# Kernel tuning notes

Measured on AMD Instinct MI355X. Metric: run time of the kernel, lower is better.

The kernel has to match this reference:

```python
import jax, jax.numpy as jnp
import numpy as np

# Architecture constants (match init_kwargs)
J_OCT, Q, K = 4, 8, 7
DECIMATION, POOLING, INDEX = 2, 8, 0
NF = K * 2 ** J_OCT            # 112 taps per filter (kernel size / time grid length)
NSC = J_OCT * Q                # 32 wavelet scales (complex filters)
POOL_W = POOLING // DECIMATION ** (INDEX + 1)  # 4


def complex_hermite_interp(xi, xk, m, p):
    # xi: (NF,) time grid; xk: (NSC, K) knots; m, p: (2, K) values/derivatives
    h = jnp.array([[1., 0., -3., 2.], [0., 1., -2., 1.],
                   [0., 0., 3., -2.], [0., 0., -1., 1.]], dtype=xi.dtype)
    xx = jnp.stack([xk[:, :-1], xk[:, 1:]], axis=2)            # (NSC, K-1, 2)
    mm = jnp.stack([m[:, :-1], m[:, 1:]], axis=2)              # (2, K-1, 2)
    pp = jnp.stack([p[:, :-1], p[:, 1:]], axis=2)
    y = jnp.concatenate([mm, pp], axis=2)                      # (2, K-1, 4)
    yh = jnp.einsum('iab,bc->iac', y, h)                       # (2, K-1, 4)
    # normalized position in each knot interval: (NSC, K-1, NF)
    xn = (xi[None, None, :] - xx[:, :, 0:1]) / (xx[:, :, 1:2] - xx[:, :, 0:1])
    mask = ((xn >= 0.) & (xn < 1.)).astype(xi.dtype)
    xp = xn[..., None] ** jnp.arange(4, dtype=xi.dtype)        # (NSC, K-1, NF, 4)
    return jnp.einsum('irf,srtf->ist', yh, xp * mask[..., None])  # (2, NSC, NF)


def get_filters(m, p, scales_delta, knots_base):
    scales = 2. ** (jnp.arange(NSC, dtype=jnp.float32) / np.float32(Q)) + scales_delta
    clipped = jnp.clip(knots_base[None, :] * scales[:, None], 1., float(NF - K))
    knots_sum = jnp.cumsum(clipped, axis=1) - clipped          # exclusive cumsum
    knots = knots_sum - (K // 2) * scales[:, None]             # (NSC, K)
    time_max = np.float32(K * 2 ** (J_OCT - 1))
    time_grid = jnp.linspace(-time_max, time_max, NF)
    mask = jnp.ones((1, K), dtype=jnp.float32).at[0, 0].set(0.).at[0, -1].set(0.)
    m_null = m - jnp.mean(m[:, 1:-1], axis=1, keepdims=True)
    f = complex_hermite_interp(time_grid, knots, m_null * mask, p * mask)  # (2, NSC, NF)
    f = f / jnp.max(f, axis=2, keepdims=True)
    filt_concat = f.reshape(2 * NSC, NF)  # [real; imag] rows, same as tf.concat axis=0
    return jnp.transpose(filt_concat)[:, None, :]              # (NF, 1, 2*NSC) = WIO


def scatter_conv(x, kernel):
    B, C, T = x.shape
    xr = x.reshape(B * C, T, 1)
    xp = jnp.pad(xr, ((0, 0), (NF // 2 - 1, NF // 2 + 1), (0, 0)), mode='symmetric')
    return jax.lax.conv_general_dilated(
        xp, kernel, window_strides=(DECIMATION,), padding='VALID',
        dimension_numbers=('NWC', 'WIO', 'NWC'))                # (B*C, To, 2*NSC)


def reference(x, m, p, scales_delta, knots_base):
    B, C, T = x.shape
    kernel = get_filters(m, p, scales_delta, knots_base)
    x_conv, vjp = jax.vjp(lambda xx: scatter_conv(xx, kernel), x)
    u = jnp.sqrt(jnp.square(x_conv[..., :NSC]) + jnp.square(x_conv[..., NSC:]))  # (B*C, To, NSC)
    out_u = jnp.swapaxes(u.reshape(B, C, NSC, -1), 1, 2)       # (B, NSC, C, To)
    pooled = jax.lax.reduce_window(u, 0., jax.lax.add,
                                   (1, POOL_W, 1), (1, POOL_W, 1), 'VALID') / POOL_W
    pooled = jnp.swapaxes(pooled, 1, 2)                        # (B*C, NSC, Tp)
    out_s = pooled.reshape(B, C, NSC, -1)                      # (B, C, NSC, Tp)
    # embedded tf.gradients auxiliary reconstruction loss
    inverse = vjp(x_conv)[0]
    loss = jnp.mean(jnp.square(inverse - jax.lax.stop_gradient(x)))
    return out_u, out_s, loss


def setup_inputs() -> dict:
    key = jax.random.key(0)
    B, C, T = 16, 3, 65536
    x = jax.random.normal(key, (B, C, T), dtype=jnp.float32)
    n = jnp.arange(K, dtype=jnp.float32)
    ham = 0.54 - 0.46 * jnp.cos(2. * jnp.pi * n / K)           # periodic hamming (tf default)
    alt = jnp.cos(n * jnp.pi) * ham
    m = jnp.stack([alt, jnp.zeros(K, jnp.float32)])
    p = jnp.stack([jnp.zeros(K, jnp.float32), alt])
    scales_delta = jnp.zeros(NSC, dtype=jnp.float32)
    knots_base = jnp.ones(K, dtype=jnp.float32)
    return {'x': x, 'm': m, 'p': p, 'scales_delta': scales_delta, 'knots_base': knots_base}
```

## Files before the change

### kernel.cpp

```cpp
#include <hip/hip_runtime.h>

#define TLEN 65536
#define XPLEN 65648
#define TO 32769
#define OU_SIZE 50333184

typedef __attribute__((ext_vector_type(8))) short short8v;
typedef __attribute__((ext_vector_type(4))) float float4v;

__device__ __forceinline__ float fetch_xp(const float* __restrict__ xr, int idx) {
    int p = idx - 55;
    p = (p < 0) ? (-1 - p) : p;
    p = (p >= TLEN) ? (2 * TLEN - 1 - p) : p;
    return xr[p];
}

__device__ __forceinline__ ushort f2bf(float f) {
    unsigned u = __float_as_uint(f);
    unsigned r = (u + 0x7fffu + ((u >> 16) & 1u)) >> 16;
    return (ushort)r;
}

__global__ __launch_bounds__(256) void k1_filters(
    const float* __restrict__ m, const float* __restrict__ p,
    const float* __restrict__ sd, const float* __restrict__ kb,
    float* __restrict__ Wout, ushort* __restrict__ Wtb)
{
    __shared__ float knots[32][8];
    __shared__ float yh[2][6][4];
    __shared__ float fv[2][32][112];
    __shared__ float mx[64];
    __shared__ float mv[2][7], pv[2][7];
    int tid = threadIdx.x;
    if (tid < 32) {
        float s = exp2f((float)tid * 0.125f) + sd[tid];
        float cum = 0.f;
        for (int k = 0; k < 7; ++k) {
            float c = fminf(fmaxf(kb[k] * s, 1.f), 105.f);
            knots[tid][k] = cum - 3.f * s;
            cum += c;
        }
    }
    if (tid < 2) {
        float mean = 0.f;
        for (int k = 1; k <= 5; ++k) mean += m[tid * 7 + k];
        mean *= 0.2f;
        for (int k = 0; k < 7; ++k) {
            float msk = (k == 0 || k == 6) ? 0.f : 1.f;
            mv[tid][k] = (m[tid * 7 + k] - mean) * msk;
            pv[tid][k] = p[tid * 7 + k] * msk;
        }
    }
    __syncthreads();
    if (tid < 12) {
        int i = tid / 6, kk = tid % 6;
        float y0 = mv[i][kk], y1 = mv[i][kk + 1], y2 = pv[i][kk], y3 = pv[i][kk + 1];
        yh[i][kk][0] = y0;
        yh[i][kk][1] = y1;
        yh[i][kk][2] = -3.f * y0 - 2.f * y1 + 3.f * y2 - y3;
        yh[i][kk][3] = 2.f * y0 + y1 - 2.f * y2 + y3;
    }
    __syncthreads();
    for (int idx = tid; idx < 7168; idx += 256) {
        int i = idx / 3584, s = (idx / 112) % 32, fi = idx % 112;
        float xi = -56.f + (float)fi * (112.f / 111.f);
        float val = 0.f;
        for (int kk = 0; kk < 6; ++kk) {
            float x0 = knots[s][kk], x1 = knots[s][kk + 1];
            float xn = (xi - x0) / (x1 - x0);
            if (xn >= 0.f && xn < 1.f) {
                val += ((yh[i][kk][3] * xn + yh[i][kk][2]) * xn + yh[i][kk][1]) * xn + yh[i][kk][0];
            }
        }
        fv[i][s][fi] = val;
    }
    __syncthreads();
    if (tid < 64) {
        int i = tid >> 5, s = tid & 31;
        float mm_ = -1e30f;
        for (int fi = 0; fi < 112; ++fi) mm_ = fmaxf(mm_, fv[i][s][fi]);
        mx[tid] = mm_;
    }
    __syncthreads();
    for (int idx = tid; idx < 7168; idx += 256) {
        int i = idx / 3584, s = (idx / 112) % 32, fi = idx % 112;
        int o = i * 32 + s;
        Wout[fi * 64 + o] = fv[i][s][fi] / mx[o];
    }
    for (int idx = tid; idx < 8192; idx += 256) {
        int o = idx >> 7, k = idx & 127;
        float val = (k < 112) ? fv[o >> 5][o & 31][k] / mx[o] : 0.f;
        Wtb[idx] = f2bf(val);
    }
}

__global__ __launch_bounds__(256) void k1b_A(const float* __restrict__ W, float* __restrict__ A)
{
    int idx = blockIdx.x * 256 + threadIdx.x;
    if (idx >= 12544) return;
    int j = idx / 112, k = idx % 112;
    float s = 0.f;
    for (int o = 0; o < 64; ++o) s += W[j * 64 + o] * W[k * 64 + o];
    A[idx] = s;
}

__global__ __launch_bounds__(256) void k1c_C(const float* __restrict__ A, float* __restrict__ C)
{
    int idx = blockIdx.x * 256 + threadIdx.x;
    if (idx >= 448) return;
    int q = idx / 224, dd = idx % 224;
    int d = dd - 111;
    float s = 0.f;
    for (int k = q; k < 112; k += 2) {
        int jj = k + d;
        if (jj >= 0 && jj < 112) s += A[jj * 112 + k];
    }
    C[idx] = s;
}

__global__ __launch_bounds__(256) void k2_fwd(
    const float* __restrict__ x, const ushort* __restrict__ Wtb,
    float* __restrict__ out_u, float* __restrict__ out_s)
{
    __shared__ __align__(16) ushort xraw[2][384];
    __shared__ float ub[256][33];
    __shared__ float pb[32][65];
    int row = blockIdx.y;
    int b = row / 3, c = row % 3;
    const float* xr = x + row * TLEN;
    int tid = threadIdx.x;
    int l = tid & 63, w = tid >> 6;
    int r16 = l & 15, kg = l >> 4;

    union U8 { short8v v; uint u[4]; uint4 q; };

    const ushort* WB = Wtb + r16 * 128 + 8 * kg;
    U8 wreg[4][4];
#pragma unroll
    for (int n = 0; n < 4; ++n)
#pragma unroll
        for (int ks = 0; ks < 4; ++ks)
            wreg[n][ks].q = *(const uint4*)(WB + n * 2048 + 32 * ks);

    int ebase = 2 * (32 * w + r16) + 8 * kg;

    int tstart = blockIdx.x * 8;
    int tend = (blockIdx.x == 31) ? 257 : (tstart + 8);

    for (int tile = tstart; tile < tend; ++tile) {
        int half = (tile - tstart) & 1;
        int t0 = tile * 128;

        for (int i = tid; i < 384; i += 256) {
            int idx = 2 * t0 + i;
            float v = (idx < XPLEN) ? fetch_xp(xr, idx) : 0.f;
            xraw[half][i] = f2bf(v);
        }
        __syncthreads();

        float4v acc[2][4];
#pragma unroll
        for (int mt = 0; mt < 2; ++mt)
#pragma unroll
            for (int n = 0; n < 4; ++n)
                acc[mt][n] = (float4v){0.f, 0.f, 0.f, 0.f};

#pragma unroll
        for (int ks = 0; ks < 4; ++ks) {
            U8 a0, a1;
            int e0 = ebase + 32 * ks;
#pragma unroll
            for (int q = 0; q < 4; ++q) {
                a0.u[q] = *(const uint*)&xraw[half][e0 + 2 * q];
                a1.u[q] = *(const uint*)&xraw[half][e0 + 32 + 2 * q];
            }
#pragma unroll
            for (int n = 0; n < 4; ++n) {
                acc[0][n] = __builtin_amdgcn_mfma_f32_16x16x32_bf16(a0.v, wreg[n][ks].v, acc[0][n], 0, 0, 0);
                acc[1][n] = __builtin_amdgcn_mfma_f32_16x16x32_bf16(a1.v, wreg[n][ks].v, acc[1][n], 0, 0, 0);
            }
        }

#pragma unroll
        for (int mt = 0; mt < 2; ++mt) {
            int tl = 32 * w + 16 * mt + 4 * kg;
            int ts = t0 + tl;
            float u1[4], u2[4];
#pragma unroll
            for (int r = 0; r < 4; ++r) {
                float re1 = acc[mt][0][r], im1 = acc[mt][2][r];
                float re2 = acc[mt][1][r], im2 = acc[mt][3][r];
                u1[r] = sqrtf(re1 * re1 + im1 * im1);
                u2[r] = sqrtf(re2 * re2 + im2 * im2);
            }
#pragma unroll
            for (int r = 0; r < 4; ++r) {
                ub[(half << 7) + tl + r][r16]      = u1[r];
                ub[(half << 7) + tl + r][r16 + 16] = u2[r];
            }
            if (ts + 3 < TO) {
                int pc = (tl >> 2) + (half << 5);
                pb[r16][pc]      = (u1[0] + u1[1] + u1[2] + u1[3]) * 0.25f;
                pb[r16 + 16][pc] = (u2[0] + u2[1] + u2[2] + u2[3]) * 0.25f;
            }
        }

        if (half || tile == tend - 1) {
            __syncthreads();
            int nt = half ? 2 : 1;
            int pend_t0 = (tile - nt + 1) * 128;
            int NE = nt << 7;

            for (int i = tid; i < (NE << 3); i += 256) {
                int r = i & 31;
                int g = i >> 5;
                size_t gb = ((size_t)((b * 32 + r) * 3 + c)) * TO + pend_t0;
                int pad = (int)((4 - (gb & 3)) & 3);
                int e = pad + (g << 2);
                if (e + 3 < NE) {
                    int t = pend_t0 + e;
                    float4 v = make_float4(ub[e][r], ub[e + 1][r], ub[e + 2][r], ub[e + 3][r]);
                    if (t + 3 < TO) {
                        *(float4*)(out_u + gb + e) = v;
                    } else {
                        if (t     < TO) out_u[gb + e]     = v.x;
                        if (t + 1 < TO) out_u[gb + e + 1] = v.y;
                        if (t + 2 < TO) out_u[gb + e + 2] = v.z;
                        if (t + 3 < TO) out_u[gb + e + 3] = v.w;
                    }
                }
            }
            if (tid < 128) {
                int r = tid >> 2, j = tid & 3;
                size_t gb = ((size_t)((b * 32 + r) * 3 + c)) * TO + pend_t0;
                int pad = (int)((4 - (gb & 3)) & 3);
                if (pad > 0) {
                    int G4 = ((NE - pad) >> 2) << 2;
                    int e = (j < pad) ? j : (pad + G4 + (j - pad));
                    if (e < NE) {
                        int t = pend_t0 + e;
                        if (t < TO) out_u[gb + e] = ub[e][r];
                    }
                }
            }
            int tp0 = pend_t0 >> 2;
            for (int i = tid; i < (nt << 8); i += 256) {
                int r = i & 31;
                int g = i >> 5;
                int tp = tp0 + (g << 2);
                size_t sb = ((size_t)(row * 32 + r)) * 8192;
                if (tp + 3 < 8192) {
                    float4 v = make_float4(pb[r][4 * g], pb[r][4 * g + 1], pb[r][4 * g + 2], pb[r][4 * g + 3]);
                    *(float4*)(out_s + sb + tp) = v;
                } else {
#pragma unroll
                    for (int j = 0; j < 4; ++j)
                        if (tp + j < 8192) out_s[sb + tp + j] = pb[r][4 * g + j];
                }
            }
        }
    }
}

__global__ __launch_bounds__(256) void k3_interior(
    const float* __restrict__ x, const float* __restrict__ C,
    double* __restrict__ part)
{
    __shared__ __align__(16) float sx[1248];
    __shared__ __align__(16) float Cl[448];
    __shared__ double wred[4];
    int row = blockIdx.y;
    int s0 = 56 + blockIdx.x * 1024;
    const float* xr = x + row * TLEN;
    int tid = threadIdx.x;
    for (int li = tid; li < 1248; li += 256) {
        int pp = s0 - 111 + li;
        pp = (pp < 0) ? (-1 - pp) : pp;
        pp = (pp >= TLEN) ? (2 * TLEN - 1 - pp) : pp;
        sx[li] = xr[pp];
    }
    for (int li = tid; li < 448; li += 256) Cl[li] = C[li];
    __syncthreads();

    int qe = (55 + s0) & 1;
    const float* Ce = Cl + qe * 224;
    const float* Co = Cl + (qe ^ 1) * 224;
    int base = tid * 4;
    float a0 = 0.f, a1 = 0.f, a2 = 0.f, a3 = 0.f;
    float4 cur = *(const float4*)&sx[base];
#pragma unroll 4
    for (int d4 = 0; d4 < 56; ++d4) {
        float4 nxt = *(const float4*)&sx[base + 4 * d4 + 4];
        float4 cev = *(const float4*)&Ce[4 * d4];
        float4 cov = *(const float4*)&Co[4 * d4];
        a0 = fmaf(cur.x, cev.x, a0); a1 = fmaf(cur.y, cov.x, a1); a2 = fmaf(cur.z, cev.x, a2); a3 = fmaf(cur.w, cov.x, a3);
        a0 = fmaf(cur.y, cev.y, a0); a1 = fmaf(cur.z, cov.y, a1); a2 = fmaf(cur.w, cev.y, a2); a3 = fmaf(nxt.x, cov.y, a3);
        a0 = fmaf(cur.z, cev.z, a0); a1 = fmaf(cur.w, cov.z, a1); a2 = fmaf(nxt.x, cev.z, a2); a3 = fmaf(nxt.y, cov.z, a3);
        a0 = fmaf(cur.w, cev.w, a0); a1 = fmaf(nxt.x, cov.w, a1); a2 = fmaf(nxt.y, cev.w, a2); a3 = fmaf(nxt.z, cov.w, a3);
        cur = nxt;
    }

    int sb = s0 + base;
    double lsum = 0.0;
    if (sb + 0 <= 65478) { float d = a0 - sx[base + 111]; lsum += (double)d * d; }
    if (sb + 1 <= 65478) { float d = a1 - sx[base + 112]; lsum += (double)d * d; }
    if (sb + 2 <= 65478) { float d = a2 - sx[base + 113]; lsum += (double)d * d; }
    if (sb + 3 <= 65478) { float d = a3 - sx[base + 114]; lsum += (double)d * d; }
    for (int off = 32; off > 0; off >>= 1) lsum += __shfl_down(lsum, off, 64);
    int w = tid >> 6;
    if ((tid & 63) == 0) wred[w] = lsum;
    __syncthreads();
    if (tid == 0)
        part[row * 64 + blockIdx.x] = wred[0] + wred[1] + wred[2] + wred[3];
}

__global__ __launch_bounds__(256) void k4_edge(
    const float* __restrict__ x, const float* __restrict__ A,
    double* __restrict__ part2)
{
    __shared__ float Al[112][113];
    __shared__ float xpw[240];
    __shared__ double wacc[4];
    int row = blockIdx.x >> 1;
    int side = blockIdx.x & 1;
    const float* xr = x + row * TLEN;
    int tid = threadIdx.x;

    for (int idx = tid; idx < 12544; idx += 256)
        Al[idx / 112][idx % 112] = A[idx];
    {
        int n_x = side ? 225 : 222;
        int woff0 = side ? 65423 : 0;
        if (tid < n_x) xpw[tid] = fetch_xp(xr, woff0 + tid);
    }
    __syncthreads();

    int w = tid >> 6, lane = tid & 63;
    int nS = side ? 57 : 56;
    int woff = side ? 65423 : 0;
    double lacc = 0.0;
    for (int s = w; s < nS; s += 4) {
        float part = 0.f;
#pragma unroll
        for (int half = 0; half < 2; ++half) {
            int i;
            bool has;
            if (!side) { i = half ? (54 - s) : (55 + s); has = half ? (s <= 54) : true; }
            else       { i = half ? (65647 - s) : (65534 + s); has = true; }
            if (has) {
                int klo = max(0, i - 65536);
                int khi = min(111, i);
                int k0 = klo + ((klo ^ i) & 1);
                for (int k = k0; k <= khi; k += 2) {
                    int bi = i - k - woff;
                    part = fmaf(xpw[bi + lane], Al[lane][k], part);
                    if (lane < 48)
                        part = fmaf(xpw[bi + 64 + lane], Al[lane + 64][k], part);
                }
            }
        }
        for (int off = 32; off > 0; off >>= 1) part += __shfl_down(part, off, 64);
        if (lane == 0) {
            float xs = xpw[side ? (111 + s) : (s + 55)];
            float diff = part - xs;
            lacc += (double)diff * diff;
        }
    }
    if (lane == 0) wacc[w] = lacc;
    __syncthreads();
    if (tid == 0) part2[blockIdx.x] = wacc[0] + wacc[1] + wacc[2] + wacc[3];
}

__global__ __launch_bounds__(256) void k5_final(
    const double* __restrict__ part, const double* __restrict__ part2,
    float* __restrict__ out_loss)
{
    __shared__ double red[256];
    double acc = 0.0;
    for (int idx = threadIdx.x; idx < 3072; idx += 256) acc += part[idx];
    if (threadIdx.x < 96) acc += part2[threadIdx.x];
    red[threadIdx.x] = acc;
    __syncthreads();
    for (int st = 128; st > 0; st >>= 1) {
        if (threadIdx.x < st) red[threadIdx.x] += red[threadIdx.x + st];
        __syncthreads();
    }
    if (threadIdx.x == 0)
        out_loss[0] = (float)(red[0] / 3145728.0);
}

extern "C" void kernel_launch(void* const* d_in, const int* in_sizes, int n_in,
                              void* d_out, int out_size, void* d_ws, size_t ws_size,
                              hipStream_t stream)
{
    (void)in_sizes; (void)n_in; (void)ws_size;
    const float* x  = (const float*)d_in[0];
    const float* m  = (const float*)d_in[1];
    const float* p  = (const float*)d_in[2];
    const float* sd = (const float*)d_in[3];
    const float* kb = (const float*)d_in[4];
    float* out = (float*)d_out;
    float* ws  = (float*)d_ws;

    float* ws_w     = ws;
    float* ws_C     = ws + 7168;
    float* ws_A     = ws + 7616;
    double* ws_part  = (double*)(ws + 20160);
    double* ws_part2 = (double*)(ws + 26304);
    ushort* ws_wtb  = (ushort*)(ws + 26496);

    k1_filters<<<1, 256, 0, stream>>>(m, p, sd, kb, ws_w, ws_wtb);
    k1b_A<<<49, 256, 0, stream>>>(ws_w, ws_A);
    k1c_C<<<2, 256, 0, stream>>>(ws_A, ws_C);
    k2_fwd<<<dim3(32, 48), 256, 0, stream>>>(x, ws_wtb, out, out + OU_SIZE);
    k3_interior<<<dim3(64, 48), 256, 0, stream>>>(x, ws_C, ws_part);
    k4_edge<<<96, 256, 0, stream>>>(x, ws_A, ws_part2);
    k5_final<<<1, 256, 0, stream>>>(ws_part, ws_part2, out + (out_size - 1));
}
```

Before: 279.7 us.

## Software-pipeline conv tile loop: prefetch next input and flush previous tile's outputs

Restructures the MFMA convolution tile loop so global loads for the next tile's input are issued before the current tile's compute. The previous tile's output stores (modulus and pooled rows) are flushed per tile, interleaved with that prefetch, rather than in bursts every two tiles. Custom LDS-only barriers with sched_barrier fences replace __syncthreads to keep the compiler from reordering across stages. The aim is to hide global load latency and spread store traffic, at the cost of more barriers per tile and smaller 128-element store batches.

```diff
diff --git a/kernel.cpp b/kernel.cpp
--- a/kernel.cpp
+++ b/kernel.cpp
@@ -19,6 +19,13 @@
     unsigned u = __float_as_uint(f);
     unsigned r = (u + 0x7fffu + ((u >> 16) & 1u)) >> 16;
     return (ushort)r;
+}
+
+__device__ __forceinline__ void bar_lds() {
+    __builtin_amdgcn_sched_barrier(0);
+    asm volatile("s_waitcnt lgkmcnt(0)" ::: "memory");
+    __builtin_amdgcn_s_barrier();
+    __builtin_amdgcn_sched_barrier(0);
 }
 
 __global__ __launch_bounds__(256) void k1_filters(
@@ -146,18 +153,99 @@
 
     int tstart = blockIdx.x * 8;
     int tend = (blockIdx.x == 31) ? 257 : (tstart + 8);
-
-    for (int tile = tstart; tile < tend; ++tile) {
-        int half = (tile - tstart) & 1;
-        int t0 = tile * 128;
-
-        for (int i = tid; i < 384; i += 256) {
-            int idx = 2 * t0 + i;
-            float v = (idx < XPLEN) ? fetch_xp(xr, idx) : 0.f;
-            xraw[half][i] = f2bf(v);
-        }
-        __syncthreads();
-
+    int ntiles = tend - tstart;
+
+    auto flush = [&](int f) {
+        int slot = (f & 1) << 7;
+        int pend_t0 = (tstart + f) * 128;
+        const int NE = 128;
+        for (int i = tid; i < (NE << 3); i += 256) {
+            int r = i & 31;
+            int g = i >> 5;
+            size_t gb = ((size_t)((b * 32 + r) * 3 + c)) * TO + pend_t0;
+            int pad = (int)((4 - (gb & 3)) & 3);
+            int e = pad + (g << 2);
+            if (e + 3 < NE) {
+                int t = pend_t0 + e;
+                float4 v = make_float4(ub[slot + e][r], ub[slot + e + 1][r],
+                                       ub[slot + e + 2][r], ub[slot + e + 3][r]);
+                if (t + 3 < TO) {
+                    *(float4*)(out_u + gb + e) = v;
+                } else {
+                    if (t     < TO) out_u[gb + e]     = v.x;
+                    if (t + 1 < TO) out_u[gb + e + 1] = v.y;
+                    if (t + 2 < TO) out_u[gb + e + 2] = v.z;
+                    if (t + 3 < TO) out_u[gb + e + 3] = v.w;
+                }
+            }
+        }
+        if (tid < 128) {
+            int r = tid >> 2, j = tid & 3;
+            size_t gb = ((size_t)((b * 32 + r) * 3 + c)) * TO + pend_t0;
+            int pad = (int)((4 - (gb & 3)) & 3);
+            if (pad > 0) {
+                int G4 = ((NE - pad) >> 2) << 2;
+                int e = (j < pad) ? j : (pad + G4 + (j - pad));
+                if (e < NE) {
+                    int t = pend_t0 + e;
+                    if (t < TO) out_u[gb + e] = ub[slot + e][r];
+                }
+            }
+        }
+        int ps = (f & 1) << 5;
+        int tp0 = pend_t0 >> 2;
+        for (int i = tid; i < 256; i += 256) {
+            int r = i & 31;
+            int g = i >> 5;
+            int tp = g << 2;
+            size_t sb = ((size_t)(row * 32 + r)) * 8192 + tp0;
+            if (tp0 + tp + 3 < 8192) {
+                float4 v = make_float4(pb[r][ps + tp], pb[r][ps + tp + 1],
+                                       pb[r][ps + tp + 2], pb[r][ps + tp + 3]);
+                *(float4*)(out_s + sb + tp) = v;
+            } else {
+#pragma unroll
+                for (int j = 0; j < 4; ++j)
+                    if (tp0 + tp + j < 8192) out_s[sb + tp + j] = pb[r][ps + tp + j];
+            }
+        }
+    };
+
+    {
+        int i0 = 2 * tstart * 128 + tid;
+        float v0 = (i0 < XPLEN) ? fetch_xp(xr, i0) : 0.f;
+        float v1 = 0.f;
+        if (tid < 128) {
+            int i1 = i0 + 256;
+            v1 = (i1 < XPLEN) ? fetch_xp(xr, i1) : 0.f;
+        }
+        xraw[0][tid] = f2bf(v0);
+        if (tid < 128) xraw[0][tid + 256] = f2bf(v1);
+    }
+    bar_lds();
+
+    for (int it = 0; it < ntiles; ++it) {
+        int half = it & 1;
+        float n0 = 0.f, n1 = 0.f;
+        bool hn = (it + 1 < ntiles);
+        if (hn) {
+            int i0 = 2 * (tstart + it + 1) * 128 + tid;
+            n0 = (i0 < XPLEN) ? fetch_xp(xr, i0) : 0.f;
+            if (tid < 128) {
+                int i1 = i0 + 256;
+                n1 = (i1 < XPLEN) ? fetch_xp(xr, i1) : 0.f;
+            }
+        }
+        __builtin_amdgcn_sched_barrier(0);
+        if (it >= 1) flush(it - 1);
+        __builtin_amdgcn_sched_barrier(0);
+        if (hn) {
+            xraw[(it + 1) & 1][tid] = f2bf(n0);
+            if (tid < 128) xraw[(it + 1) & 1][tid + 256] = f2bf(n1);
+        }
+        bar_lds();
+
+        const ushort* xcur = xraw[half];
         float4v acc[2][4];
 #pragma unroll
         for (int mt = 0; mt < 2; ++mt)
@@ -171,8 +259,8 @@
             int e0 = ebase + 32 * ks;
 #pragma unroll
             for (int q = 0; q < 4; ++q) {
-                a0.u[q] = *(const uint*)&xraw[half][e0 + 2 * q];
-                a1.u[q] = *(const uint*)&xraw[half][e0 + 32 + 2 * q];
+                a0.u[q] = *(const uint*)&xcur[e0 + 2 * q];
+                a1.u[q] = *(const uint*)&xcur[e0 + 32 + 2 * q];
             }
 #pragma unroll
             for (int n = 0; n < 4; ++n) {
@@ -181,6 +269,7 @@
             }
         }
 
+        int t0 = (tstart + it) * 128;
 #pragma unroll
         for (int mt = 0; mt < 2; ++mt) {
             int tl = 32 * w + 16 * mt + 4 * kg;
@@ -199,67 +288,14 @@
                 ub[(half << 7) + tl + r][r16 + 16] = u2[r];
             }
             if (ts + 3 < TO) {
-                int pc = (tl >> 2) + (half << 5);
+                int pc = (half << 5) + (tl >> 2);
                 pb[r16][pc]      = (u1[0] + u1[1] + u1[2] + u1[3]) * 0.25f;
                 pb[r16 + 16][pc] = (u2[0] + u2[1] + u2[2] + u2[3]) * 0.25f;
             }
         }
-
-        if (half || tile == tend - 1) {
-            __syncthreads();
-            int nt = half ? 2 : 1;
-            int pend_t0 = (tile - nt + 1) * 128;
-            int NE = nt << 7;
-
-            for (int i = tid; i < (NE << 3); i += 256) {
-                int r = i & 31;
-                int g = i >> 5;
-                size_t gb = ((size_t)((b * 32 + r) * 3 + c)) * TO + pend_t0;
-                int pad = (int)((4 - (gb & 3)) & 3);
-                int e = pad + (g << 2);
-                if (e + 3 < NE) {
-                    int t = pend_t0 + e;
-                    float4 v = make_float4(ub[e][r], ub[e + 1][r], ub[e + 2][r], ub[e + 3][r]);
-                    if (t + 3 < TO) {
-                        *(float4*)(out_u + gb + e) = v;
-                    } else {
-                        if (t     < TO) out_u[gb + e]     = v.x;
-                        if (t + 1 < TO) out_u[gb + e + 1] = v.y;
-                        if (t + 2 < TO) out_u[gb + e + 2] = v.z;
-                        if (t + 3 < TO) out_u[gb + e + 3] = v.w;
-                    }
-                }
-            }
-            if (tid < 128) {
-                int r = tid >> 2, j = tid & 3;
-                size_t gb = ((size_t)((b * 32 + r) * 3 + c)) * TO + pend_t0;
-                int pad = (int)((4 - (gb & 3)) & 3);
-                if (pad > 0) {
-                    int G4 = ((NE - pad) >> 2) << 2;
-                    int e = (j < pad) ? j : (pad + G4 + (j - pad));
-                    if (e < NE) {
-                        int t = pend_t0 + e;
-                        if (t < TO) out_u[gb + e] = ub[e][r];
-                    }
-                }
-            }
-            int tp0 = pend_t0 >> 2;
-            for (int i = tid; i < (nt << 8); i += 256) {
-                int r = i & 31;
-                int g = i >> 5;
-                int tp = tp0 + (g << 2);
-                size_t sb = ((size_t)(row * 32 + r)) * 8192;
-                if (tp + 3 < 8192) {
-                    float4 v = make_float4(pb[r][4 * g], pb[r][4 * g + 1], pb[r][4 * g + 2], pb[r][4 * g + 3]);
-                    *(float4*)(out_s + sb + tp) = v;
-                } else {
-#pragma unroll
-                    for (int j = 0; j < 4; ++j)
-                        if (tp + j < 8192) out_s[sb + tp + j] = pb[r][4 * g + j];
-                }
-            }
-        }
-    }
+        bar_lds();
+    }
+    flush(ntiles - 1);
 }
 
 __global__ __launch_bounds__(256) void k3_interior(
```

Measured after the change: 273.7 us. 2.1% less time.
